# Kernel tuning notes

Measured on AMD Instinct MI355X. Metric: run time of the kernel, lower is better.

Reference implementation:

```python
import jax, jax.numpy as jnp
import numpy as np

EPS = 1e-4

def mp_weight(w):
    # MP_GeoLinear eval-mode weight: normalize then scale by gain/sqrt(fan_in)
    w32 = w.astype(jnp.float32)
    norm = jnp.linalg.norm(w32, axis=1, keepdims=True)          # [out,1]
    fan_in = w.shape[1]
    denom = EPS + norm / np.sqrt(fan_in)                        # torch.add(eps, norm, alpha=sqrt(1/fan_in))
    wn = w32 / denom
    return (wn / np.sqrt(fan_in)).astype(w.dtype)               # gain=1


def setup_inputs() -> dict:
    key = jax.random.key(0)
    k1, k2, k3, k4 = jax.random.split(key, 4)
    N, E, C = 100000, 1600000, 128
    x = jax.random.normal(k1, (N, C), dtype=jnp.float32)
    edge_index = jax.random.randint(k2, (2, E), 0, N, dtype=jnp.int64)
    w_neigh = jax.random.normal(k3, (C, C), dtype=jnp.float32)
    w_res = jax.random.normal(k4, (C, C), dtype=jnp.float32)
    return {"x": x, "edge_index": edge_index, "w_neigh": w_neigh, "w_res": w_res}


def reference(x, edge_index, w_neigh, w_res):
    N = x.shape[0]
    row, col = edge_index[0], edge_index[1]            # source, target
    # degree of target nodes
    deg = jax.ops.segment_sum(jnp.ones_like(col, dtype=x.dtype), col, num_segments=N)
    deg_inv = jnp.where(deg > 0, deg ** -0.5, 0.0)     # inf -> 0
    norm = deg_inv[col]                                 # [E]
    # message: x_j * norm, aggregate: scatter-add into col
    msg = x[row] * norm[:, None]                        # [E,C]
    agg = jax.ops.segment_sum(msg, col, num_segments=N) # [N,C]
    neighbourhood = agg @ mp_weight(w_neigh).T
    residual = x @ mp_weight(w_res).T
    # mp_sum(residual, neighbourhood, t=0.5) = (a+b)/sqrt(2)
    join = (residual + neighbourhood) / np.sqrt(2.0)
    out = jnp.where((deg > 0)[:, None], join, residual)
    return out
```

## Files before the change

### kernel.cpp

```cpp
#include <hip/hip_runtime.h>
#include <hip/hip_bf16.h>

#define C 128
#define INV_SQRT2 0.7071067811865476f
#define NB 1024
#define BS 128
#define EPB 4096
#define NXCD 8
#define SUBCAP 384
#define LIDX_CAP 4096
#define AGS 68
#define GSTRIDE 16

typedef __attribute__((ext_vector_type(8))) short short8;
typedef __attribute__((ext_vector_type(4))) float f32x4;

__device__ inline ushort f2b(float f) {
    __hip_bfloat16 h = __float2bfloat16(f);
    return __builtin_bit_cast(ushort, h);
}


__global__ __launch_bounds__(512) void k_front(
    const int* __restrict__ row, const int* __restrict__ col, int E, int nblk,
    int* __restrict__ gcursor, unsigned int* __restrict__ recs,
    const float4* __restrict__ x, ushort* __restrict__ xb, int n4, int castBlocks,
    const float* __restrict__ w_res, const float* __restrict__ w_neigh,
    ushort* __restrict__ Bp)
{
    __shared__ int hist[NB];
    __shared__ int lbase[NB];
    int b = blockIdx.x;
    int t = threadIdx.x;
    if (b < nblk) {
        unsigned int rec0[EPB / 512];
        unsigned int key0[EPB / 512];
        hist[t] = 0; hist[t + 512] = 0;
        __syncthreads();
        int base = b * EPB;
        #pragma unroll
        for (int i = 0; i < EPB / 512; i++) {
            int e = base + i * 512 + t;
            if (e < E) {
                int c = col[e];
                int kk = c >> 7;
                int r = atomicAdd(&hist[kk], 1);
                rec0[i] = ((unsigned int)(c & 127) << 24) | (unsigned int)row[e];
                key0[i] = (unsigned int)kk | ((unsigned int)r << 10);
            } else {
                key0[i] = 0xFFFFFFFFu;
            }
        }
        __syncthreads();
        int xcd = b & 7;
        int* gc = gcursor + (size_t)xcd * NB * GSTRIDE;
        #pragma unroll
        for (int kx = 0; kx < 2; kx++) {
            int bb = t + kx * 512;
            int h = hist[bb];
            lbase[bb] = h ? atomicAdd(&gc[bb * GSTRIDE], h) : 0;
        }
        __syncthreads();
        #pragma unroll
        for (int i = 0; i < EPB / 512; i++) {
            unsigned int key = key0[i];
            if (key != 0xFFFFFFFFu) {
                int kk = (int)(key & 1023u);
                int p = lbase[kk] + (int)(key >> 10);
                if (p < SUBCAP)
                    recs[((size_t)kk * NXCD + xcd) * SUBCAP + p] = rec0[i];
            }
        }
    } else if (b < nblk + castBlocks) {
        int i0 = (b - nblk) * 2048 + t;
        #pragma unroll
        for (int u = 0; u < 4; u++) {
            int i = i0 + u * 512;
            if (i < n4) {
                float4 v = x[i];
                ushort4 o;
                o.x = f2b(v.x); o.y = f2b(v.y); o.z = f2b(v.z); o.w = f2b(v.w);
                *(ushort4*)(xb + (size_t)i * 4) = o;
            }
        }
        if (b == nblk && t < 32) {
            ushort4 z = make_ushort4(0, 0, 0, 0);
            *(ushort4*)(xb + ((size_t)n4 << 2) + (t << 2)) = z;
        }
    } else {
        int r = (b - nblk - castBlocks) * 8 + (t >> 6);
        int h = r >> 7;
        int i = r & 127;
        const float* w = h ? w_neigh : w_res;
        int lane = t & 63;
        float a = w[i * C + lane];
        float bb = w[i * C + lane + 64];
        float ss = a * a + bb * bb;
        #pragma unroll
        for (int off = 32; off > 0; off >>= 1) ss += __shfl_down(ss, off);
        ss = __shfl(ss, 0);
        float norm = sqrtf(ss);
        float denom = 1e-4f + norm * 0.08838834764831845f;
        float scale = 1.0f / (denom * 11.313708498984761f);
        int c1 = lane, c2 = lane + 64;
        Bp[(size_t)(h * 16 + (c1 >> 3)) * 1024 + i * 8 + (c1 & 7)] = f2b(a * scale);
        Bp[(size_t)(h * 16 + (c2 >> 3)) * 1024 + i * 8 + (c2 & 7)] = f2b(bb * scale);
    }
}


#define ACCUM(v) do { \
    acc[0] += __builtin_bit_cast(float, (v).x << 16); \
    acc[1] += __builtin_bit_cast(float, (v).x & 0xffff0000u); \
    acc[2] += __builtin_bit_cast(float, (v).y << 16); \
    acc[3] += __builtin_bit_cast(float, (v).y & 0xffff0000u); \
    acc[4] += __builtin_bit_cast(float, (v).z << 16); \
    acc[5] += __builtin_bit_cast(float, (v).z & 0xffff0000u); \
    acc[6] += __builtin_bit_cast(float, (v).w << 16); \
    acc[7] += __builtin_bit_cast(float, (v).w & 0xffff0000u); \
} while (0)

__global__ __launch_bounds__(512, 8) void k_fused(
    const unsigned int* __restrict__ recs, const int* __restrict__ gcursor,
    const ushort* __restrict__ xb, const ushort* __restrict__ Bp,
    int* __restrict__ lidxg, float* __restrict__ out, int N, int kofs)
{
    __shared__ int shist[BS];
    __shared__ int sexcl[BS];
    __shared__ int scur[BS];
    __shared__ int scnt8[NXCD];
    __shared__ uint sAgg[BS * AGS];

    int k = blockIdx.x + kofs;
    int t = threadIdx.x;
    const unsigned int* rb = recs + (size_t)k * NXCD * SUBCAP;
    int* lw = lidxg + (size_t)k * LIDX_CAP;

    if (t < NXCD) {
        int c0 = gcursor[((size_t)t * NB + k) * GSTRIDE];
        scnt8[t] = (c0 > SUBCAP) ? SUBCAP : c0;
    }
    if (t < BS) shist[t] = 0;
    __syncthreads();
    #pragma unroll 1
    for (int xx = 0; xx < NXCD; xx++) {
        int cx = scnt8[xx];
        for (int i = t; i < cx; i += 512)
            atomicAdd(&shist[rb[xx * SUBCAP + i] >> 24], 1);
    }
    __syncthreads();
    if (t < 64) {
        int a = shist[t], bb = shist[t + 64];
        int pa = (a + 7) & ~7, pb = (bb + 7) & ~7;
        int ia = pa, ib = pb;
        #pragma unroll
        for (int off = 1; off < 64; off <<= 1) {
            int ya = __shfl_up(ia, off);
            int yb = __shfl_up(ib, off);
            if (t >= off) { ia += ya; ib += yb; }
        }
        int tot0 = __shfl(ia, 63);
        int e0 = ia - pa;
        int e1 = ib - pb + tot0;
        sexcl[t] = e0;      scur[t] = e0;
        sexcl[t + 64] = e1; scur[t + 64] = e1;
    }
    __syncthreads();
    #pragma unroll 1
    for (int xx = 0; xx < NXCD; xx++) {
        int cx = scnt8[xx];
        for (int i = t; i < cx; i += 512) {
            unsigned int r = rb[xx * SUBCAP + i];
            int c = r >> 24;
            int p = atomicAdd(&scur[c], 1);
            lw[p] = (int)(r & 0xFFFFFF);
        }
    }
    if (t < BS) {
        int d = shist[t], b0 = sexcl[t];
        int pe = b0 + ((d + 7) & ~7);
        for (int p = b0 + d; p < pe; p++) lw[p] = N;
    }
    __syncthreads();

    int lane = t & 63;
    int wave = t >> 6;
    int s  = lane >> 4;
    int cl = lane & 15;
    const ushort* xcl = xb + (cl << 3);
    #pragma unroll 1
    for (int ln = wave * 16; ln < wave * 16 + 16; ln++) {
        int j  = sexcl[ln];
        int d  = shist[ln];
        int jend = j + ((d + 7) & ~7);
        float acc[8];
        #pragma unroll
        for (int i = 0; i < 8; i++) acc[i] = 0.f;
        for (; j + 16 <= jend; j += 16) {
            int i0 = lw[j + s];
            int i1 = lw[j + 4 + s];
            int i2 = lw[j + 8 + s];
            int i3 = lw[j + 12 + s];
            uint4 va = *(const uint4*)(xcl + ((size_t)i0 << 7));
            uint4 vb = *(const uint4*)(xcl + ((size_t)i1 << 7));
            uint4 vc = *(const uint4*)(xcl + ((size_t)i2 << 7));
            uint4 vd = *(const uint4*)(xcl + ((size_t)i3 << 7));
            ACCUM(va);
            ACCUM(vb);
            ACCUM(vc);
            ACCUM(vd);
        }
        if (j < jend) {
            int i0 = lw[j + s];
            int i1 = lw[j + 4 + s];
            uint4 va = *(const uint4*)(xcl + ((size_t)i0 << 7));
            uint4 vb = *(const uint4*)(xcl + ((size_t)i1 << 7));
            ACCUM(va);
            ACCUM(vb);
        }
        #pragma unroll
        for (int i = 0; i < 8; i++) {
            acc[i] += __shfl_xor(acc[i], 16);
            acc[i] += __shfl_xor(acc[i], 32);
        }
        float dd = (d > 0) ? rsqrtf((float)d) : 0.f;
        if (lane < 16) {
            uint4 o;
            o.x = (uint)f2b(acc[0] * dd) | ((uint)f2b(acc[1] * dd) << 16);
            o.y = (uint)f2b(acc[2] * dd) | ((uint)f2b(acc[3] * dd) << 16);
            o.z = (uint)f2b(acc[4] * dd) | ((uint)f2b(acc[5] * dd) << 16);
            o.w = (uint)f2b(acc[6] * dd) | ((uint)f2b(acc[7] * dd) << 16);
            *(uint4*)&sAgg[ln * AGS + cl * 4] = o;
        }
    }
    asm volatile("s_waitcnt lgkmcnt(0)" ::: "memory");

    int quad = lane >> 4;
    int l16  = lane & 15;
    long gbase = (long)k * BS;
    int arow = wave * 16 + l16;
    long garow = gbase + arow;
    if (garow >= N) garow = N - 1;

    f32x4 oacc[8];
    #pragma unroll
    for (int nt = 0; nt < 8; nt++) oacc[nt] = (f32x4){0.f, 0.f, 0.f, 0.f};

    #pragma unroll
    for (int kk = 0; kk < 8; kk++) {
        short8 af;
        if (kk < 4) {
            af = *(const short8*)(xb + garow * C + kk * 32 + quad * 8);
        } else {
            af = *(const short8*)&sAgg[arow * AGS + (kk - 4) * 16 + quad * 4];
        }
        #pragma unroll
        for (int nt = 0; nt < 8; nt++) {
            short8 bf = *(const short8*)(Bp +
                ((size_t)((kk * 4 + quad) * 128) + nt * 16 + l16) * 8);
            oacc[nt] = __builtin_amdgcn_mfma_f32_16x16x32_bf16(af, bf, oacc[nt], 0, 0, 0);
        }
    }

    #pragma unroll
    for (int r2 = 0; r2 < 4; r2++) {
        int rl = wave * 16 + quad * 4 + r2;
        long rowg = gbase + rl;
        if (rowg < N) {
            float sc = (shist[rl] > 0) ? INV_SQRT2 : 1.0f;
            float* o = out + rowg * C + l16;
            #pragma unroll
            for (int nt = 0; nt < 8; nt++)
                __builtin_nontemporal_store(oacc[nt][r2] * sc, &o[nt * 16]);
        }
    }
}


extern "C" void kernel_launch(void* const* d_in, const int* in_sizes, int n_in,
                              void* d_out, int out_size, void* d_ws, size_t ws_size,
                              hipStream_t stream) {
    const float* x       = (const float*)d_in[0];
    const int*   eidx    = (const int*)d_in[1];
    const float* w_neigh = (const float*)d_in[2];
    const float* w_res   = (const float*)d_in[3];
    float* out = (float*)d_out;

    int N = in_sizes[0] / C;
    int E = in_sizes[1] / 2;
    const int* row = eidx;
    const int* col = eidx + E;

    char* ws = (char*)d_ws;
    size_t off = 0;
    auto alloc = [&](size_t bytes) {
        size_t o = off;
        off += (bytes + 511) & ~(size_t)511;
        return o;
    };
    int nblk = (E + EPB - 1) / EPB;

    int*    gcursor    = (int*)(ws + alloc((size_t)NXCD * NB * GSTRIDE * 4));
    unsigned int* recs = (unsigned int*)(ws + alloc((size_t)NB * NXCD * SUBCAP * 4));
    ushort* Bp         = (ushort*)(ws + alloc((size_t)32 * 1024 * 2));
    ushort* xb         = (ushort*)(ws + alloc((size_t)N * C * 2 + 65536));
    int*    lidxg      = (int*)(ws + alloc((size_t)NB * LIDX_CAP * 4));
    (void)ws_size;

    hipMemsetAsync(gcursor, 0, (size_t)NXCD * NB * GSTRIDE * 4, stream);

    int nbuckets = (N + BS - 1) / BS;
    int n4 = N * C / 4;
    int castBlocks = (n4 + 2047) / 2048;

    k_front<<<nblk + castBlocks + 32, 512, 0, stream>>>(
        row, col, E, nblk, gcursor, recs,
        (const float4*)x, xb, n4, castBlocks, w_res, w_neigh, Bp);

    int half = (nbuckets + 1) / 2;
    k_fused<<<half, 512, 0, stream>>>(recs, gcursor, xb, Bp, lidxg, out, N, 0);
    if (nbuckets - half > 0)
        k_fused<<<nbuckets - half, 512, 0, stream>>>(recs, gcursor, xb, Bp, lidxg,
                                                     out, N, half);
}
```

Before: 225.7 us.

## Use two-pass bucket histogram with larger edge chunks and single fused launch

The binning kernel now processes 16384 edges per block instead of 4096. It first counts bucket histograms, then reserves global slots, then re-reads col/row and scatters records using a second shared-memory atomic pass. Records are no longer held in registers, so fewer blocks issue global cursor atomics and register pressure drops, at the cost of reading col twice. The two half-grid k_fused launches are merged into one, removing launch overhead.

```diff
diff --git a/kernel.cpp b/kernel.cpp
--- a/kernel.cpp
+++ b/kernel.cpp
@@ -5,7 +5,7 @@
 #define INV_SQRT2 0.7071067811865476f
 #define NB 1024
 #define BS 128
-#define EPB 4096
+#define EPB 16384
 #define NXCD 8
 #define SUBCAP 384
 #define LIDX_CAP 4096
@@ -33,42 +33,36 @@
     int b = blockIdx.x;
     int t = threadIdx.x;
     if (b < nblk) {
-        unsigned int rec0[EPB / 512];
-        unsigned int key0[EPB / 512];
         hist[t] = 0; hist[t + 512] = 0;
         __syncthreads();
         int base = b * EPB;
-        #pragma unroll
+        #pragma unroll 4
+        for (int i = 0; i < EPB / 512; i++) {
+            int e = base + i * 512 + t;
+            if (e < E) atomicAdd(&hist[col[e] >> 7], 1);
+        }
+        __syncthreads();
+        int xcd = b & 7;
+        int* gc = gcursor + (size_t)xcd * NB * GSTRIDE;
+        #pragma unroll
+        for (int kx = 0; kx < 2; kx++) {
+            int bb = t + kx * 512;
+            int h = hist[bb];
+            lbase[bb] = h ? atomicAdd(&gc[bb * GSTRIDE], h) : 0;
+        }
+        __syncthreads();
+        hist[t] = 0; hist[t + 512] = 0;
+        __syncthreads();
+        #pragma unroll 4
         for (int i = 0; i < EPB / 512; i++) {
             int e = base + i * 512 + t;
             if (e < E) {
                 int c = col[e];
                 int kk = c >> 7;
-                int r = atomicAdd(&hist[kk], 1);
-                rec0[i] = ((unsigned int)(c & 127) << 24) | (unsigned int)row[e];
-                key0[i] = (unsigned int)kk | ((unsigned int)r << 10);
-            } else {
-                key0[i] = 0xFFFFFFFFu;
-            }
-        }
-        __syncthreads();
-        int xcd = b & 7;
-        int* gc = gcursor + (size_t)xcd * NB * GSTRIDE;
-        #pragma unroll
-        for (int kx = 0; kx < 2; kx++) {
-            int bb = t + kx * 512;
-            int h = hist[bb];
-            lbase[bb] = h ? atomicAdd(&gc[bb * GSTRIDE], h) : 0;
-        }
-        __syncthreads();
-        #pragma unroll
-        for (int i = 0; i < EPB / 512; i++) {
-            unsigned int key = key0[i];
-            if (key != 0xFFFFFFFFu) {
-                int kk = (int)(key & 1023u);
-                int p = lbase[kk] + (int)(key >> 10);
+                int p = atomicAdd(&hist[kk], 1) + lbase[kk];
                 if (p < SUBCAP)
-                    recs[((size_t)kk * NXCD + xcd) * SUBCAP + p] = rec0[i];
+                    recs[((size_t)kk * NXCD + xcd) * SUBCAP + p] =
+                        ((unsigned int)(c & 127) << 24) | (unsigned int)row[e];
             }
         }
     } else if (b < nblk + castBlocks) {
@@ -123,7 +117,7 @@
 __global__ __launch_bounds__(512, 8) void k_fused(
     const unsigned int* __restrict__ recs, const int* __restrict__ gcursor,
     const ushort* __restrict__ xb, const ushort* __restrict__ Bp,
-    int* __restrict__ lidxg, float* __restrict__ out, int N, int kofs)
+    int* __restrict__ lidxg, float* __restrict__ out, int N)
 {
     __shared__ int shist[BS];
     __shared__ int sexcl[BS];
@@ -131,7 +125,7 @@
     __shared__ int scnt8[NXCD];
     __shared__ uint sAgg[BS * AGS];
 
-    int k = blockIdx.x + kofs;
+    int k = blockIdx.x;
     int t = threadIdx.x;
     const unsigned int* rb = recs + (size_t)k * NXCD * SUBCAP;
     int* lw = lidxg + (size_t)k * LIDX_CAP;
@@ -307,7 +301,7 @@
     int*    lidxg      = (int*)(ws + alloc((size_t)NB * LIDX_CAP * 4));
     (void)ws_size;
 
-    hipMemsetAsync(gcursor, 0, (size_t)NXCD * NB * GSTRIDE * 4, stream);
+    (void)hipMemsetAsync(gcursor, 0, (size_t)NXCD * NB * GSTRIDE * 4, stream);
 
     int nbuckets = (N + BS - 1) / BS;
     int n4 = N * C / 4;
@@ -316,10 +310,5 @@
     k_front<<<nblk + castBlocks + 32, 512, 0, stream>>>(
         row, col, E, nblk, gcursor, recs,
         (const float4*)x, xb, n4, castBlocks, w_res, w_neigh, Bp);
-
-    int half = (nbuckets + 1) / 2;
-    k_fused<<<half, 512, 0, stream>>>(recs, gcursor, xb, Bp, lidxg, out, N, 0);
-    if (nbuckets - half > 0)
-        k_fused<<<nbuckets - half, 512, 0, stream>>>(recs, gcursor, xb, Bp, lidxg,
-                                                     out, N, half);
+    k_fused<<<nbuckets, 512, 0, stream>>>(recs, gcursor, xb, Bp, lidxg, out, N);
 }
```

Measured after the change: 235.9 us. 1.04x slower.
